# Optimization experiments

Measured on AMD Instinct MI355X. Metric: run time of the kernel, lower is better.

Reference implementation:

```python
import jax, jax.numpy as jnp
import numpy as np

EPS_LOG = 1e-08   # module's eps added inside the log
EPS_PD = 1e-06    # torch.nn.PairwiseDistance default eps (added to the difference)


def setup_inputs() -> dict:
    key = jax.random.key(0)
    x = jax.random.normal(key, (16384, 512), dtype=jnp.float32)
    return {"x": x}


def reference(x):
    n = x.shape[0]
    # Pairwise dot products; mask diagonal with -1 (as in the torch code)
    dots = jnp.matmul(x, x.T)  # [n, n]
    dots = jnp.where(jnp.eye(n, dtype=bool), jnp.float32(-1.0), dots)
    I = jnp.argmax(dots, axis=1)  # nearest neighbor index per row (no grad)
    # torch PairwiseDistance(2): ||x1 - x2 + eps||_2 with eps=1e-6
    diff = x - x[I] + EPS_PD  # [n, d]
    rho = jnp.sqrt(jnp.sum(diff * diff, axis=1))  # [n]
    loss = -jnp.mean(jnp.log(rho + EPS_LOG))
    return loss
```

## Files before the change

kernel.cpp:

```cpp
#include <hip/hip_runtime.h>
#include <stdint.h>

#define N_ROWS 16384
#define DIM    512

typedef float v4f __attribute__((ext_vector_type(4)));
typedef unsigned long long u64;
typedef unsigned char u8;

__device__ __forceinline__ unsigned fkey(float f) {
    unsigned u = __float_as_uint(f);
    return (u & 0x80000000u) ? ~u : (u | 0x80000000u);
}

__device__ __forceinline__ void gload_lds16(const void* g, void* l) {
    __builtin_amdgcn_global_load_lds(
        (const __attribute__((address_space(1))) unsigned int*)g,
        (__attribute__((address_space(3))) unsigned int*)l,
        16, 0, 0);
}

__global__ __launch_bounds__(256)
void convert_fp8_kernel(const float* __restrict__ x, unsigned* __restrict__ x8,
                        u64* __restrict__ table) {
    int tid    = blockIdx.x * blockDim.x + threadIdx.x;
    int stride = gridDim.x * blockDim.x;
    if (tid < N_ROWS) table[tid] = 0;
    const float4* x4 = (const float4*)x;
    const int n4 = (N_ROWS * DIM) / 4;
    for (int i = tid; i < n4; i += stride) {
        float4 v = x4[i];
        int b = __builtin_amdgcn_cvt_pk_fp8_f32(v.x, v.y, 0, false);
        b     = __builtin_amdgcn_cvt_pk_fp8_f32(v.z, v.w, b, true);
        x8[i] = (unsigned)b;
    }
}

__global__ __launch_bounds__(256)
void argmax_dots_kernel(const u8* __restrict__ xb, u64* __restrict__ table) {
    __shared__ __attribute__((aligned(16))) u8 ldsA[128 * 128];
    __shared__ __attribute__((aligned(16))) u8 ldsB[128 * 128];

    const int u = blockIdx.x >> 6;
    const int p = blockIdx.x & 63;
    const int rT = (u <= p) ? (127 - p) : p;
    const int cT = (u <= p) ? (127 - u) : (u - 1);

    const int t      = threadIdx.x;
    const int lane   = t & 63;
    const int wave   = t >> 6;
    const int lane15 = lane & 15;
    const int quad   = lane >> 4;
    const int rh = wave >> 1;
    const int ch = wave & 1;

    const int rowBase = rT * 128;
    const int colBase = cT * 128;

    const u8* gA[4];
    const u8* gB[4];
#pragma unroll
    for (int j = 0; j < 4; ++j) {
        const int L   = j * 256 + t;
        const int row = L >> 3;
        const int kc  = (L & 7) ^ (row & 7);
        gA[j] = xb + (size_t)(rowBase + row) * DIM + kc * 16;
        gB[j] = xb + (size_t)(colBase + row) * DIM + kc * 16;
    }
    const int dstOff = wave * 1024;

    const int aBase = (rh * 64 + lane15) * 128 + (quad & 1) * 8;
    const int bBase = (ch * 64 + lane15) * 128 + (quad & 1) * 8;
    int xorK[4];
#pragma unroll
    for (int s = 0; s < 4; ++s)
        xorK[s] = ((2 * s + (quad >> 1)) ^ (lane15 & 7)) << 4;

    v4f acc[4][4];
#pragma unroll
    for (int rf = 0; rf < 4; ++rf)
#pragma unroll
        for (int cf = 0; cf < 4; ++cf) {
            v4f z = {0.f, 0.f, 0.f, 0.f};
            acc[rf][cf] = z;
        }

#pragma unroll
    for (int k = 0; k < 4; ++k) {
        const int kk = k * 128;
#pragma unroll
        for (int j = 0; j < 4; ++j) {
            gload_lds16(gA[j] + kk, (char*)ldsA + j * 4096 + dstOff);
            gload_lds16(gB[j] + kk, (char*)ldsB + j * 4096 + dstOff);
        }
        __syncthreads();

#pragma unroll
        for (int s = 0; s < 4; ++s) {
            const int xs = xorK[s];
            long a8[4], b8[4];
#pragma unroll
            for (int rf = 0; rf < 4; ++rf)
                a8[rf] = *(const long*)(ldsA + aBase + rf * 2048 + xs);
#pragma unroll
            for (int cf = 0; cf < 4; ++cf)
                b8[cf] = *(const long*)(ldsB + bBase + cf * 2048 + xs);
#pragma unroll
            for (int rf = 0; rf < 4; ++rf)
#pragma unroll
                for (int cf = 0; cf < 4; ++cf)
                    acc[rf][cf] = __builtin_amdgcn_mfma_f32_16x16x32_fp8_fp8(
                        a8[rf], b8[cf], acc[rf][cf], 0, 0, 0);
        }
        __syncthreads();
    }

    const int colLane = colBase + ch * 64 + lane15;
#pragma unroll
    for (int rf = 0; rf < 4; ++rf) {
#pragma unroll
        for (int e = 0; e < 4; ++e) {
            const int row = rowBase + rh * 64 + rf * 16 + quad * 4 + e;
            float bv = -3.0e38f;
            int   bc = 0;
#pragma unroll
            for (int cf = 0; cf < 4; ++cf) {
                const float v = acc[rf][cf][e];
                const int col = colLane + cf * 16;
                if (v > bv && col != row) { bv = v; bc = col; }
            }
            u64 packed = ((u64)fkey(bv) << 32) | (unsigned)(~bc);
#pragma unroll
            for (int m = 1; m < 16; m <<= 1) {
                u64 o = __shfl_xor(packed, m, 64);
                if (o > packed) packed = o;
            }
            if (lane15 == 0) atomicMax(&table[row], packed);
        }
    }

    if (rT != cT) {
#pragma unroll
        for (int cf = 0; cf < 4; ++cf) {
            const int col = colLane + cf * 16;
            float bv = -3.0e38f;
            int   br_ = 0;
#pragma unroll
            for (int rf = 0; rf < 4; ++rf)
#pragma unroll
                for (int e = 0; e < 4; ++e) {
                    const float v = acc[rf][cf][e];
                    const int row = rowBase + rh * 64 + rf * 16 + quad * 4 + e;
                    if (v > bv) { bv = v; br_ = row; }
                }
            u64 packed = ((u64)fkey(bv) << 32) | (unsigned)(~br_);
            u64 o = __shfl_xor(packed, 16, 64); if (o > packed) packed = o;
            o     = __shfl_xor(packed, 32, 64); if (o > packed) packed = o;
            if (quad == 0) atomicMax(&table[col], packed);
        }
    }
}

__global__ __launch_bounds__(256)
void rho_loss_kernel(const float* __restrict__ x, const u64* __restrict__ table,
                     float* __restrict__ out) {
    const int lane = threadIdx.x & 63;
    const int wave = threadIdx.x >> 6;
    const int waveGlobal = blockIdx.x * 4 + wave;

    float local = 0.f;
    for (int r8 = 0; r8 < 8; ++r8) {
        const int row = waveGlobal * 8 + r8;
        const u64 packed = table[row];
        const int nb = (int)(~(unsigned)(packed & 0xFFFFFFFFu));

        const float4* xr = (const float4*)(x + (size_t)row * DIM);
        const float4* xn = (const float4*)(x + (size_t)nb  * DIM);
        float s = 0.f;
#pragma unroll
        for (int tt = 0; tt < 2; ++tt) {
            float4 a = xr[lane * 2 + tt];
            float4 b = xn[lane * 2 + tt];
            float d0 = a.x - b.x + 1e-6f;
            float d1 = a.y - b.y + 1e-6f;
            float d2 = a.z - b.z + 1e-6f;
            float d3 = a.w - b.w + 1e-6f;
            s += d0 * d0 + d1 * d1 + d2 * d2 + d3 * d3;
        }
#pragma unroll
        for (int m = 1; m < 64; m <<= 1) s += __shfl_xor(s, m, 64);

        if (lane == 0) {
            float rho = sqrtf(s);
            local += logf(rho + 1e-8f);
        }
    }
    if (lane == 0) atomicAdd(out, -local * (1.0f / 16384.0f));
}

extern "C" void kernel_launch(void* const* d_in, const int* in_sizes, int n_in,
                              void* d_out, int out_size, void* d_ws, size_t ws_size,
                              hipStream_t stream) {
    const float* x = (const float*)d_in[0];

    u8*    xb    = (u8*)d_ws;
    u64*   table = (u64*)((char*)d_ws + (size_t)N_ROWS * DIM);
    float* out   = (float*)d_out;

    hipMemsetAsync(out, 0, sizeof(float), stream);

    convert_fp8_kernel<<<2048, 256, 0, stream>>>(x, (unsigned*)xb, table);
    argmax_dots_kernel<<<8256, 256, 0, stream>>>(xb, table);
    rho_loss_kernel<<<512, 256, 0, stream>>>(x, table, out);
}
```

Measured before the change: 263.1 us.

## Switch fp8 MFMA from 16x16x32 to 32x32x16 tiles and fold output memset

After: 381.3 us. 44.9% more time.

```diff
diff --git a/kernel.cpp b/kernel.cpp
--- a/kernel.cpp
+++ b/kernel.cpp
@@ -4,7 +4,7 @@
 #define N_ROWS 16384
 #define DIM    512
 
-typedef float v4f __attribute__((ext_vector_type(4)));
+typedef float v16f __attribute__((ext_vector_type(16)));
 typedef unsigned long long u64;
 typedef unsigned char u8;
 
@@ -22,10 +22,11 @@
 
 __global__ __launch_bounds__(256)
 void convert_fp8_kernel(const float* __restrict__ x, unsigned* __restrict__ x8,
-                        u64* __restrict__ table) {
+                        u64* __restrict__ table, float* __restrict__ out) {
     int tid    = blockIdx.x * blockDim.x + threadIdx.x;
     int stride = gridDim.x * blockDim.x;
     if (tid < N_ROWS) table[tid] = 0;
+    if (tid == 0) out[0] = 0.f;
     const float4* x4 = (const float4*)x;
     const int n4 = (N_ROWS * DIM) / 4;
     for (int i = tid; i < n4; i += stride) {
@@ -46,11 +47,11 @@
     const int rT = (u <= p) ? (127 - p) : p;
     const int cT = (u <= p) ? (127 - u) : (u - 1);
 
-    const int t      = threadIdx.x;
-    const int lane   = t & 63;
-    const int wave   = t >> 6;
-    const int lane15 = lane & 15;
-    const int quad   = lane >> 4;
+    const int t    = threadIdx.x;
+    const int lane = t & 63;
+    const int wave = t >> 6;
+    const int l31  = lane & 31;
+    const int h    = lane >> 5;
     const int rh = wave >> 1;
     const int ch = wave & 1;
 
@@ -69,21 +70,19 @@
     }
     const int dstOff = wave * 1024;
 
-    const int aBase = (rh * 64 + lane15) * 128 + (quad & 1) * 8;
-    const int bBase = (ch * 64 + lane15) * 128 + (quad & 1) * 8;
-    int xorK[4];
-#pragma unroll
-    for (int s = 0; s < 4; ++s)
-        xorK[s] = ((2 * s + (quad >> 1)) ^ (lane15 & 7)) << 4;
-
-    v4f acc[4][4];
-#pragma unroll
-    for (int rf = 0; rf < 4; ++rf)
-#pragma unroll
-        for (int cf = 0; cf < 4; ++cf) {
-            v4f z = {0.f, 0.f, 0.f, 0.f};
-            acc[rf][cf] = z;
-        }
+    const int e7 = l31 & 7;
+    const int aOff0 = (rh * 64 + l31) * 128 + h * 8;
+    const int aOff1 = aOff0 + 32 * 128;
+    const int bOff0 = (ch * 64 + l31) * 128 + h * 8;
+    const int bOff1 = bOff0 + 32 * 128;
+
+    v16f acc[2][2];
+#pragma unroll
+    for (int rf = 0; rf < 2; ++rf)
+#pragma unroll
+        for (int cf = 0; cf < 2; ++cf)
+#pragma unroll
+            for (int e = 0; e < 16; ++e) acc[rf][cf][e] = 0.f;
 
 #pragma unroll
     for (int k = 0; k < 4; ++k) {
@@ -96,67 +95,61 @@
         __syncthreads();
 
 #pragma unroll
-        for (int s = 0; s < 4; ++s) {
-            const int xs = xorK[s];
-            long a8[4], b8[4];
-#pragma unroll
-            for (int rf = 0; rf < 4; ++rf)
-                a8[rf] = *(const long*)(ldsA + aBase + rf * 2048 + xs);
-#pragma unroll
-            for (int cf = 0; cf < 4; ++cf)
-                b8[cf] = *(const long*)(ldsB + bBase + cf * 2048 + xs);
-#pragma unroll
-            for (int rf = 0; rf < 4; ++rf)
-#pragma unroll
-                for (int cf = 0; cf < 4; ++cf)
-                    acc[rf][cf] = __builtin_amdgcn_mfma_f32_16x16x32_fp8_fp8(
-                        a8[rf], b8[cf], acc[rf][cf], 0, 0, 0);
+        for (int s = 0; s < 8; ++s) {
+            const int xs = ((s ^ e7) << 4);
+            long a0 = *(const long*)(ldsA + aOff0 + xs);
+            long a1 = *(const long*)(ldsA + aOff1 + xs);
+            long b0 = *(const long*)(ldsB + bOff0 + xs);
+            long b1 = *(const long*)(ldsB + bOff1 + xs);
+            acc[0][0] = __builtin_amdgcn_mfma_f32_32x32x16_fp8_fp8(a0, b0, acc[0][0], 0, 0, 0);
+            acc[0][1] = __builtin_amdgcn_mfma_f32_32x32x16_fp8_fp8(a0, b1, acc[0][1], 0, 0, 0);
+            acc[1][0] = __builtin_amdgcn_mfma_f32_32x32x16_fp8_fp8(a1, b0, acc[1][0], 0, 0, 0);
+            acc[1][1] = __builtin_amdgcn_mfma_f32_32x32x16_fp8_fp8(a1, b1, acc[1][1], 0, 0, 0);
         }
         __syncthreads();
     }
 
-    const int colLane = colBase + ch * 64 + lane15;
-#pragma unroll
-    for (int rf = 0; rf < 4; ++rf) {
-#pragma unroll
-        for (int e = 0; e < 4; ++e) {
-            const int row = rowBase + rh * 64 + rf * 16 + quad * 4 + e;
+#pragma unroll
+    for (int rf = 0; rf < 2; ++rf) {
+#pragma unroll
+        for (int reg = 0; reg < 16; ++reg) {
+            const int row = rowBase + rh * 64 + rf * 32 + (reg & 3) + 8 * (reg >> 2) + 4 * h;
             float bv = -3.0e38f;
             int   bc = 0;
 #pragma unroll
-            for (int cf = 0; cf < 4; ++cf) {
-                const float v = acc[rf][cf][e];
-                const int col = colLane + cf * 16;
+            for (int cf = 0; cf < 2; ++cf) {
+                const float v = acc[rf][cf][reg];
+                const int col = colBase + ch * 64 + cf * 32 + l31;
                 if (v > bv && col != row) { bv = v; bc = col; }
             }
             u64 packed = ((u64)fkey(bv) << 32) | (unsigned)(~bc);
 #pragma unroll
-            for (int m = 1; m < 16; m <<= 1) {
+            for (int m = 1; m < 32; m <<= 1) {
                 u64 o = __shfl_xor(packed, m, 64);
                 if (o > packed) packed = o;
             }
-            if (lane15 == 0) atomicMax(&table[row], packed);
+            if (l31 == 0) atomicMax(&table[row], packed);
         }
     }
 
     if (rT != cT) {
 #pragma unroll
-        for (int cf = 0; cf < 4; ++cf) {
-            const int col = colLane + cf * 16;
+        for (int cf = 0; cf < 2; ++cf) {
+            const int col = colBase + ch * 64 + cf * 32 + l31;
             float bv = -3.0e38f;
             int   br_ = 0;
 #pragma unroll
-            for (int rf = 0; rf < 4; ++rf)
-#pragma unroll
-                for (int e = 0; e < 4; ++e) {
-                    const float v = acc[rf][cf][e];
-                    const int row = rowBase + rh * 64 + rf * 16 + quad * 4 + e;
+            for (int rf = 0; rf < 2; ++rf)
+#pragma unroll
+                for (int reg = 0; reg < 16; ++reg) {
+                    const float v = acc[rf][cf][reg];
+                    const int row = rowBase + rh * 64 + rf * 32 + (reg & 3) + 8 * (reg >> 2) + 4 * h;
                     if (v > bv) { bv = v; br_ = row; }
                 }
             u64 packed = ((u64)fkey(bv) << 32) | (unsigned)(~br_);
-            u64 o = __shfl_xor(packed, 16, 64); if (o > packed) packed = o;
-            o     = __shfl_xor(packed, 32, 64); if (o > packed) packed = o;
-            if (quad == 0) atomicMax(&table[col], packed);
+            u64 o = __shfl_xor(packed, 32, 64);
+            if (o > packed) packed = o;
+            if (h == 0) atomicMax(&table[col], packed);
         }
     }
 }
@@ -207,9 +200,7 @@
     u64*   table = (u64*)((char*)d_ws + (size_t)N_ROWS * DIM);
     float* out   = (float*)d_out;
 
-    hipMemsetAsync(out, 0, sizeof(float), stream);
-
-    convert_fp8_kernel<<<2048, 256, 0, stream>>>(x, (unsigned*)xb, table);
+    convert_fp8_kernel<<<2048, 256, 0, stream>>>(x, (unsigned*)xb, table, out);
     argmax_dots_kernel<<<8256, 256, 0, stream>>>(xb, table);
     rho_loss_kernel<<<512, 256, 0, stream>>>(x, table, out);
 }
```

## Switch Gram argmax to int8 MFMA with fragment-ordered LDS layout

Applied to the files above, without the earlier changes.

New measurement: 266.4 us. Within noise of the previous version (+1.3%).

```diff
diff --git a/kernel.cpp b/kernel.cpp
--- a/kernel.cpp
+++ b/kernel.cpp
@@ -4,14 +4,9 @@
 #define N_ROWS 16384
 #define DIM    512
 
-typedef float v4f __attribute__((ext_vector_type(4)));
+typedef int v4i __attribute__((ext_vector_type(4)));
 typedef unsigned long long u64;
 typedef unsigned char u8;
-
-__device__ __forceinline__ unsigned fkey(float f) {
-    unsigned u = __float_as_uint(f);
-    return (u & 0x80000000u) ? ~u : (u | 0x80000000u);
-}
 
 __device__ __forceinline__ void gload_lds16(const void* g, void* l) {
     __builtin_amdgcn_global_load_lds(
@@ -21,18 +16,21 @@
 }
 
 __global__ __launch_bounds__(256)
-void convert_fp8_kernel(const float* __restrict__ x, unsigned* __restrict__ x8,
-                        u64* __restrict__ table) {
+void convert_i8_kernel(const float* __restrict__ x, unsigned* __restrict__ x8,
+                       u64* __restrict__ table, float* __restrict__ out) {
     int tid    = blockIdx.x * blockDim.x + threadIdx.x;
     int stride = gridDim.x * blockDim.x;
     if (tid < N_ROWS) table[tid] = 0;
+    if (tid == 0) out[0] = 0.f;
     const float4* x4 = (const float4*)x;
     const int n4 = (N_ROWS * DIM) / 4;
     for (int i = tid; i < n4; i += stride) {
         float4 v = x4[i];
-        int b = __builtin_amdgcn_cvt_pk_fp8_f32(v.x, v.y, 0, false);
-        b     = __builtin_amdgcn_cvt_pk_fp8_f32(v.z, v.w, b, true);
-        x8[i] = (unsigned)b;
+        int a = (int)rintf(fminf(fmaxf(v.x * 31.75f, -127.f), 127.f));
+        int b = (int)rintf(fminf(fmaxf(v.y * 31.75f, -127.f), 127.f));
+        int c = (int)rintf(fminf(fmaxf(v.z * 31.75f, -127.f), 127.f));
+        int d = (int)rintf(fminf(fmaxf(v.w * 31.75f, -127.f), 127.f));
+        x8[i] = (unsigned)((a & 0xFF) | ((b & 0xFF) << 8) | ((c & 0xFF) << 16) | (d << 24));
     }
 }
 
@@ -61,27 +59,20 @@
     const u8* gB[4];
 #pragma unroll
     for (int j = 0; j < 4; ++j) {
-        const int L   = j * 256 + t;
-        const int row = L >> 3;
-        const int kc  = (L & 7) ^ (row & 7);
+        const int G   = j * 256 + t;
+        const int row = ((G >> 9) << 6) + (((G >> 6) & 3) << 4) + (G & 15);
+        const int kc  = (((G >> 8) & 1) << 2) + ((G >> 4) & 3);
         gA[j] = xb + (size_t)(rowBase + row) * DIM + kc * 16;
         gB[j] = xb + (size_t)(colBase + row) * DIM + kc * 16;
     }
     const int dstOff = wave * 1024;
 
-    const int aBase = (rh * 64 + lane15) * 128 + (quad & 1) * 8;
-    const int bBase = (ch * 64 + lane15) * 128 + (quad & 1) * 8;
-    int xorK[4];
-#pragma unroll
-    for (int s = 0; s < 4; ++s)
-        xorK[s] = ((2 * s + (quad >> 1)) ^ (lane15 & 7)) << 4;
-
-    v4f acc[4][4];
+    v4i acc[4][4];
 #pragma unroll
     for (int rf = 0; rf < 4; ++rf)
 #pragma unroll
         for (int cf = 0; cf < 4; ++cf) {
-            v4f z = {0.f, 0.f, 0.f, 0.f};
+            v4i z = {0, 0, 0, 0};
             acc[rf][cf] = z;
         }
 
@@ -96,20 +87,19 @@
         __syncthreads();
 
 #pragma unroll
-        for (int s = 0; s < 4; ++s) {
-            const int xs = xorK[s];
-            long a8[4], b8[4];
+        for (int s = 0; s < 2; ++s) {
+            v4i a8[4], b8[4];
 #pragma unroll
             for (int rf = 0; rf < 4; ++rf)
-                a8[rf] = *(const long*)(ldsA + aBase + rf * 2048 + xs);
+                a8[rf] = *(const v4i*)(ldsA + rh * 8192 + s * 4096 + rf * 1024 + lane * 16);
 #pragma unroll
             for (int cf = 0; cf < 4; ++cf)
-                b8[cf] = *(const long*)(ldsB + bBase + cf * 2048 + xs);
+                b8[cf] = *(const v4i*)(ldsB + ch * 8192 + s * 4096 + cf * 1024 + lane * 16);
 #pragma unroll
             for (int rf = 0; rf < 4; ++rf)
 #pragma unroll
                 for (int cf = 0; cf < 4; ++cf)
-                    acc[rf][cf] = __builtin_amdgcn_mfma_f32_16x16x32_fp8_fp8(
+                    acc[rf][cf] = __builtin_amdgcn_mfma_i32_16x16x64_i8(
                         a8[rf], b8[cf], acc[rf][cf], 0, 0, 0);
         }
         __syncthreads();
@@ -121,15 +111,15 @@
 #pragma unroll
         for (int e = 0; e < 4; ++e) {
             const int row = rowBase + rh * 64 + rf * 16 + quad * 4 + e;
-            float bv = -3.0e38f;
-            int   bc = 0;
+            int bv = -2147483647;
+            int bc = 0;
 #pragma unroll
             for (int cf = 0; cf < 4; ++cf) {
-                const float v = acc[rf][cf][e];
+                const int v = acc[rf][cf][e];
                 const int col = colLane + cf * 16;
                 if (v > bv && col != row) { bv = v; bc = col; }
             }
-            u64 packed = ((u64)fkey(bv) << 32) | (unsigned)(~bc);
+            u64 packed = ((u64)((unsigned)bv ^ 0x80000000u) << 32) | (unsigned)(~bc);
 #pragma unroll
             for (int m = 1; m < 16; m <<= 1) {
                 u64 o = __shfl_xor(packed, m, 64);
@@ -143,17 +133,17 @@
 #pragma unroll
         for (int cf = 0; cf < 4; ++cf) {
             const int col = colLane + cf * 16;
-            float bv = -3.0e38f;
-            int   br_ = 0;
+            int bv = -2147483647;
+            int br_ = 0;
 #pragma unroll
             for (int rf = 0; rf < 4; ++rf)
 #pragma unroll
                 for (int e = 0; e < 4; ++e) {
-                    const float v = acc[rf][cf][e];
+                    const int v = acc[rf][cf][e];
                     const int row = rowBase + rh * 64 + rf * 16 + quad * 4 + e;
                     if (v > bv) { bv = v; br_ = row; }
                 }
-            u64 packed = ((u64)fkey(bv) << 32) | (unsigned)(~br_);
+            u64 packed = ((u64)((unsigned)bv ^ 0x80000000u) << 32) | (unsigned)(~br_);
             u64 o = __shfl_xor(packed, 16, 64); if (o > packed) packed = o;
             o     = __shfl_xor(packed, 32, 64); if (o > packed) packed = o;
             if (quad == 0) atomicMax(&table[col], packed);
@@ -207,9 +197,7 @@
     u64*   table = (u64*)((char*)d_ws + (size_t)N_ROWS * DIM);
     float* out   = (float*)d_out;
 
-    hipMemsetAsync(out, 0, sizeof(float), stream);
-
-    convert_fp8_kernel<<<2048, 256, 0, stream>>>(x, (unsigned*)xb, table);
+    convert_i8_kernel<<<2048, 256, 0, stream>>>(x, (unsigned*)xb, table, out);
     argmax_dots_kernel<<<8256, 256, 0, stream>>>(xb, table);
     rho_loss_kernel<<<512, 256, 0, stream>>>(x, table, out);
 }
```
